# Performance work log

Hardware: AMD Instinct MI355X
Metric: run time of the kernel (lower is better)

Reference implementation:

```python
import jax, jax.numpy as jnp
import numpy as np

B, D, ND, N2, H = 16384, 512, 4, 32, 4
C = D  # attention channels (per-detector feature dim)
EPS = 1e-5


def setup_inputs() -> dict:
    key = jax.random.key(0)
    ks = jax.random.split(key, 8)
    rn = lambda k, s, sc: jax.random.normal(k, s, jnp.float32) * sc
    return {
        'x': jax.random.normal(ks[0], (B, D), jnp.float32),
        'bn1_g': jnp.ones(D * ND, jnp.float32), 'bn1_b': jnp.zeros(D * ND, jnp.float32),
        'w1': rn(ks[1], (ND, D, D), 1e-4),  # diagonal blocks of the masked EnsembleLinear weight
        'bn2_g': jnp.ones(D * ND, jnp.float32), 'bn2_b': jnp.zeros(D * ND, jnp.float32),
        'wq': rn(ks[2], (C, D), 0.02), 'bq': jnp.zeros(C, jnp.float32),
        'wk': rn(ks[3], (C, D), 0.02), 'bk': jnp.zeros(C, jnp.float32),
        'wv': rn(ks[4], (C, D), 0.02), 'bv': jnp.zeros(C, jnp.float32),
        'wo': rn(ks[5], (C, C), 0.02), 'bo': jnp.zeros(C, jnp.float32),
        'ln1_g': jnp.ones(C, jnp.float32), 'ln1_b': jnp.zeros(C, jnp.float32),
        'wff': rn(ks[6], (C, C), 0.02), 'bff': jnp.zeros(C, jnp.float32),
        'ln2_g': jnp.ones(C, jnp.float32), 'ln2_b': jnp.zeros(C, jnp.float32),
        'w2': rn(ks[7], (ND, N2, D), 1e-4),
        'bn3_g': jnp.ones(N2 * ND, jnp.float32), 'bn3_b': jnp.zeros(N2 * ND, jnp.float32),
    }


def _batchnorm(x, g, b):
    # training-mode BatchNorm1d: biased batch stats over the batch axis
    m = x.mean(0)
    v = ((x - m) ** 2).mean(0)
    return (x - m) * jax.lax.rsqrt(v + EPS) * g + b


def _layernorm(x, g, b):
    m = x.mean(-1, keepdims=True)
    v = ((x - m) ** 2).mean(-1, keepdims=True)
    return (x - m) * jax.lax.rsqrt(v + EPS) * g + b


def reference(x, bn1_g, bn1_b, w1, bn2_g, bn2_b, wq, bq, wk, bk, wv, bv, wo, bo,
              ln1_g, ln1_b, wff, bff, ln2_g, ln2_b, w2, bn3_g, bn3_b):
    n = x.shape[0]
    # concat x num_detectors times along features: [n, ND*D]
    xc = jnp.tile(x, (1, ND))
    h = _batchnorm(xc, bn1_g, bn1_b)
    # EnsembleLinear 1: block-diagonal masked matmul == one small GEMM per detector
    h = jnp.einsum('ndi,doi->ndo', h.reshape(n, ND, D), w1).reshape(n, ND * D)
    h = jax.nn.sigmoid(_batchnorm(h, bn2_g, bn2_b))
    # 4-token self-attention over detectors: t is [n, ND, D]
    t = h.reshape(n, ND, D)
    hd = C // H
    q = (t @ wq.T + bq).reshape(n, ND, H, hd).transpose(0, 2, 1, 3)  # [n,H,S,hd]
    k = (t @ wk.T + bk).reshape(n, ND, H, hd).transpose(0, 2, 1, 3)
    v = (t @ wv.T + bv).reshape(n, ND, H, hd).transpose(0, 2, 1, 3)
    scale = jnp.sqrt(jnp.float32(C / H))
    scores = jnp.einsum('nhqd,nhkd->nhqk', q, k) / scale
    attn = jax.nn.softmax(scores, axis=-1)
    o = jnp.einsum('nhqk,nhkd->nhqd', attn, v).transpose(0, 2, 1, 3).reshape(n, ND, C)
    o = o @ wo.T + bo
    a1 = _layernorm(o + t, ln1_g, ln1_b)
    a2 = _layernorm(a1 @ wff.T + bff + a1, ln2_g, ln2_b)
    # EnsembleLinear 2: per-detector D -> N2
    h2 = jnp.einsum('ndi,doi->ndo', a2, w2).reshape(n, ND * N2)
    out = jax.nn.sigmoid(_batchnorm(h2, bn3_g, bn3_b))
    return out
```

## Files before the change

kernel.cpp:

```cpp
#include <hip/hip_runtime.h>
#include <hip/hip_bf16.h>

#define EPS 1e-5f

typedef __attribute__((ext_vector_type(8))) short bf16x8;
typedef __attribute__((ext_vector_type(4))) float f32x4;
typedef __attribute__((ext_vector_type(4))) float float4v;

__device__ __forceinline__ float b2f(short u) {
    union { unsigned int i; float f; } x;
    x.i = ((unsigned int)(unsigned short)u) << 16;
    return x.f;
}
__device__ __forceinline__ short f2b(float f) {
    unsigned int x = __builtin_bit_cast(unsigned int, f);
    unsigned int r = (x + 0x7FFFu + ((x >> 16) & 1u)) >> 16;
    return (short)r;
}

__device__ __forceinline__ void load_lds16(const void* g, void* l) {
    __builtin_amdgcn_global_load_lds(
        (const __attribute__((address_space(1))) unsigned int*)g,
        (__attribute__((address_space(3))) unsigned int*)l, 16, 0, 0);
}


__global__ __launch_bounds__(256) void k_cast_bf16(const float* __restrict__ src,
                                                   short* __restrict__ dst, int n8) {
    int i = blockIdx.x * 256 + threadIdx.x;
    if (i >= n8) return;
    const float4v* s = (const float4v*)src;
    float4v a = s[(long)i * 2], b = s[(long)i * 2 + 1];
    bf16x8 o;
    o[0] = f2b(a[0]); o[1] = f2b(a[1]); o[2] = f2b(a[2]); o[3] = f2b(a[3]);
    o[4] = f2b(b[0]); o[5] = f2b(b[1]); o[6] = f2b(b[2]); o[7] = f2b(b[3]);
    *(bf16x8*)(dst + (long)i * 8) = o;
}

__global__ void k_concat3(const float* __restrict__ a, const float* __restrict__ b,
                          const float* __restrict__ c, float* __restrict__ dst) {
    int i = blockIdx.x * 256 + threadIdx.x;
    if (i < 512) dst[i] = a[i];
    else if (i < 1024) dst[i] = b[i - 512];
    else if (i < 1536) dst[i] = c[i - 1024];
}

__global__ __launch_bounds__(256) void k_statcast_x(const float* __restrict__ x,
                                                    short* __restrict__ xb,
                                                    float* __restrict__ psum, float* __restrict__ psq) {
    int b = blockIdx.x, tid = threadIdx.x;
    const float* xp = x + (long)b * 64 * 512;
    short* xo = xb + (long)b * 64 * 512;
    float s0 = 0, q0 = 0, s1 = 0, q1 = 0;
    for (int r = 0; r < 64; ++r) {
        float v0 = xp[r * 512 + tid];
        float v1 = xp[r * 512 + tid + 256];
        xo[r * 512 + tid] = f2b(v0);
        xo[r * 512 + tid + 256] = f2b(v1);
        s0 += v0; q0 += v0 * v0; s1 += v1; q1 += v1 * v1;
    }
    psum[b * 512 + tid] = s0; psum[b * 512 + tid + 256] = s1;
    psq[b * 512 + tid] = q0;  psq[b * 512 + tid + 256] = q1;
}


__global__ __launch_bounds__(256) void k_finalize_meanrs(const float* __restrict__ psum,
                                                         const float* __restrict__ psq,
                                                         int nparts, int ncols, float invB,
                                                         float* __restrict__ mean, float* __restrict__ rs) {
    int l = threadIdx.x & 63, grp = threadIdx.x >> 6;
    int c = blockIdx.x * 64 + l;
    float s = 0, q = 0;
    for (int p = grp; p < nparts; p += 4) {
        s += psum[(long)p * ncols + c];
        q += psq[(long)p * ncols + c];
    }
    __shared__ float rs_[4][64], rq_[4][64];
    rs_[grp][l] = s; rq_[grp][l] = q;
    __syncthreads();
    if (grp == 0) {
        s = rs_[0][l] + rs_[1][l] + rs_[2][l] + rs_[3][l];
        q = rq_[0][l] + rq_[1][l] + rq_[2][l] + rq_[3][l];
        float m = s * invB;
        float v = q * invB - m * m;
        mean[c] = m;
        rs[c] = rsqrtf(v + EPS);
    }
}

__global__ __launch_bounds__(256) void k_finalize_ss(const float* __restrict__ psum,
                                                     const float* __restrict__ psq,
                                                     int nparts, int ncols, float invB,
                                                     const float* __restrict__ g, const float* __restrict__ bb,
                                                     float* __restrict__ scale, float* __restrict__ shift) {
    int l = threadIdx.x & 63, grp = threadIdx.x >> 6;
    int c = blockIdx.x * 64 + l;
    float s = 0, q = 0;
    for (int p = grp; p < nparts; p += 4) {
        s += psum[(long)p * ncols + c];
        q += psq[(long)p * ncols + c];
    }
    __shared__ float rs_[4][64], rq_[4][64];
    rs_[grp][l] = s; rq_[grp][l] = q;
    __syncthreads();
    if (grp == 0) {
        s = rs_[0][l] + rs_[1][l] + rs_[2][l] + rs_[3][l];
        q = rq_[0][l] + rq_[1][l] + rq_[2][l] + rq_[3][l];
        float m = s * invB, v = q * invB - m * m;
        float sc = g[c] * rsqrtf(v + EPS);
        scale[c] = sc;
        shift[c] = bb[c] - m * sc;
    }
}

__global__ __launch_bounds__(256) void k_fold_w1(const float* __restrict__ w1, const float* __restrict__ g1,
                                                 const float* __restrict__ b1, const float* __restrict__ mean,
                                                 const float* __restrict__ rs,
                                                 short* __restrict__ W1b, float* __restrict__ beff) {
    int bx = blockIdx.x;
    int d = bx >> 9, tid = threadIdx.x;
    const float* wrow = w1 + (long)bx * 512;
    float part = 0.f;
    for (int i = tid; i < 512; i += 256) {
        float wv = wrow[i];
        float sc = rs[i] * g1[d * 512 + i];
        W1b[(long)bx * 512 + i] = f2b(wv * sc);
        part += (b1[d * 512 + i] - mean[i] * sc) * wv;
    }
    __shared__ float red[256];
    red[tid] = part;
    __syncthreads();
    for (int st = 128; st > 0; st >>= 1) {
        if (tid < st) red[tid] += red[tid + st];
        __syncthreads();
    }
    if (tid == 0) beff[bx] = red[0];
}

__global__ __launch_bounds__(256) void k_bnsig(const short* h, short* t,
                                               const float* __restrict__ scale,
                                               const float* __restrict__ shift) {
    long i8 = ((long)blockIdx.x * 256 + threadIdx.x) * 8;
    int c0 = (int)(i8 & 2047);
    bf16x8 v = *(const bf16x8*)(h + i8);
    bf16x8 o;
#pragma unroll
    for (int j = 0; j < 8; ++j) {
        float x = b2f(v[j]) * scale[c0 + j] + shift[c0 + j];
        o[j] = f2b(1.f / (1.f + __expf(-x)));
    }
    *(bf16x8*)(t + i8) = o;
}

__global__ __launch_bounds__(256) void k_ln(const short* in, short* out,
                                            const float* __restrict__ g, const float* __restrict__ bb) {
    int w = threadIdx.x >> 6, lane = threadIdx.x & 63;
    long row = (long)blockIdx.x * 4 + w;
    const short* rp = in + row * 512;
    bf16x8 v = *(const bf16x8*)(rp + lane * 8);
    float f[8];
    float s = 0.f;
#pragma unroll
    for (int j = 0; j < 8; ++j) { f[j] = b2f(v[j]); s += f[j]; }
#pragma unroll
    for (int m = 1; m < 64; m <<= 1) s += __shfl_xor(s, m, 64);
    float mean = s * (1.f / 512.f);
    float q = 0.f;
#pragma unroll
    for (int j = 0; j < 8; ++j) { float d = f[j] - mean; q += d * d; }
#pragma unroll
    for (int m = 1; m < 64; m <<= 1) q += __shfl_xor(q, m, 64);
    float rs = rsqrtf(q * (1.f / 512.f) + EPS);
    bf16x8 o;
#pragma unroll
    for (int j = 0; j < 8; ++j) {
        int c = lane * 8 + j;
        o[j] = f2b((f[j] - mean) * rs * g[c] + bb[c]);
    }
    *(bf16x8*)(out + row * 512 + lane * 8) = o;
}

__global__ __launch_bounds__(256) void k_stats_o(const float* __restrict__ pre,
                                                 float* __restrict__ psum, float* __restrict__ psq) {
    int b = blockIdx.x, tid = threadIdx.x;
    int c = tid & 127, rh = tid >> 7;
    const float* pp = pre + (long)b * 128 * 128;
    float s = 0, q = 0;
    for (int r = rh; r < 128; r += 2) {
        float v = pp[r * 128 + c];
        s += v; q += v * v;
    }
    psum[(b * 2 + rh) * 128 + c] = s;
    psq[(b * 2 + rh) * 128 + c] = q;
}

__global__ __launch_bounds__(256) void k_bn3sig(const float* __restrict__ pre, float* __restrict__ out,
                                                const float* __restrict__ scale, const float* __restrict__ shift) {
    long i4 = ((long)blockIdx.x * 256 + threadIdx.x) * 4;
    float4v v = *(const float4v*)(pre + i4);
    int c0 = (int)(i4 & 127);
    float4v o;
#pragma unroll
    for (int j = 0; j < 4; ++j) {
        float x = v[j] * scale[c0 + j] + shift[c0 + j];
        o[j] = 1.f / (1.f + __expf(-x));
    }
    *(float4v*)(out + i4) = o;
}


template <int BM, int BN, int WGM, int WGN, bool ADD_RES, bool OUT_BF16>
__global__ __launch_bounds__(WGM* WGN * 64) void k_gemm_bt(
    const short* __restrict__ A, int a_zoff, int lda,
    const short* __restrict__ W, int w_zoff,
    const float* __restrict__ bias, int bias_zoff,
    short* __restrict__ Cb, float* __restrict__ Cf, int c_zoff, int ldc,
    const short* __restrict__ R, int ldr, int K) {
    constexpr int BK = 32;
    constexpr int WM = BM / WGM, WN = BN / WGN;
    constexpr int AM = WM / 16, AN = WN / 16;
    constexpr int NT = WGM * WGN * 64;
    constexpr int CH = (BM + BN) * (BK / 8);

    __shared__ alignas(16) short Smem[(BM + BN) * BK];

    int tid = threadIdx.x;
    int wave = tid >> 6, lane = tid & 63;
    int wm = (wave % WGM) * WM, wn = (wave / WGM) * WN;
    long m0 = (long)blockIdx.x * BM;
    int n0 = blockIdx.y * BN;
    int z = blockIdx.z;
    const short* Az = A + (long)z * a_zoff;
    const short* Wz = W + (long)z * w_zoff;

    f32x4 acc[AM][AN];
#pragma unroll
    for (int i = 0; i < AM; ++i)
#pragma unroll
        for (int j = 0; j < AN; ++j)
#pragma unroll
            for (int q = 0; q < 4; ++q) acc[i][j][q] = 0.f;

    int fr = lane & 15, ko = (lane >> 4) * 8;

    for (int k0 = 0; k0 < K; k0 += BK) {
#pragma unroll
        for (int c = tid; c < CH; c += NT) {
            int row = c >> 2, koff = (c & 3) * 8;
            const short* g = (row < BM) ? (Az + (m0 + row) * lda + k0 + koff)
                                        : (Wz + (long)(n0 + row - BM) * K + k0 + koff);
            load_lds16(g, (char*)Smem + (size_t)c * 16);
        }
        __syncthreads();
        bf16x8 af[AM], bfr[AN];
#pragma unroll
        for (int i = 0; i < AM; ++i) af[i] = *(const bf16x8*)(&Smem[(wm + i * 16 + fr) * BK + ko]);
#pragma unroll
        for (int j = 0; j < AN; ++j) bfr[j] = *(const bf16x8*)(&Smem[(BM + wn + j * 16 + fr) * BK + ko]);
#pragma unroll
        for (int i = 0; i < AM; ++i)
#pragma unroll
            for (int j = 0; j < AN; ++j)
                acc[i][j] = __builtin_amdgcn_mfma_f32_16x16x32_bf16(af[i], bfr[j], acc[i][j], 0, 0, 0);
        __syncthreads();
    }

    int cr = (lane >> 4) * 4, cc = lane & 15;
#pragma unroll
    for (int i = 0; i < AM; ++i) {
#pragma unroll
        for (int j = 0; j < AN; ++j) {
            int col = n0 + wn + j * 16 + cc;
            float bv = bias ? bias[(long)z * bias_zoff + col] : 0.f;
#pragma unroll
            for (int q = 0; q < 4; ++q) {
                long row = m0 + wm + i * 16 + cr + q;
                float v = acc[i][j][q] + bv;
                if constexpr (ADD_RES) v += b2f(R[row * (long)ldr + col]);
                long idx = row * (long)ldc + (long)z * c_zoff + col;
                if constexpr (OUT_BF16) Cb[idx] = f2b(v);
                else Cf[idx] = v;
            }
        }
    }
}


__global__ __launch_bounds__(256) void k_gemm_e1(
    const short* __restrict__ A, const short* __restrict__ W1, const float* __restrict__ beff,
    short* __restrict__ h, float* __restrict__ psum, float* __restrict__ psq) {
    constexpr int BK = 32;
    __shared__ alignas(16) short Smem[256 * BK];
    __shared__ float cS[2][128], cQ[2][128];

    int tid = threadIdx.x;
    int wave = tid >> 6, lane = tid & 63;
    int wm = (wave & 1) * 64, wn = (wave >> 1) * 64;
    long m0 = (long)blockIdx.x * 128;
    int n0 = blockIdx.y * 128;
    int z = blockIdx.z;
    const short* Wz = W1 + (long)z * 512 * 512;

    f32x4 acc[4][4];
#pragma unroll
    for (int i = 0; i < 4; ++i)
#pragma unroll
        for (int j = 0; j < 4; ++j)
#pragma unroll
            for (int q = 0; q < 4; ++q) acc[i][j][q] = 0.f;

    int fr = lane & 15, ko = (lane >> 4) * 8;

    for (int k0 = 0; k0 < 512; k0 += BK) {
#pragma unroll
        for (int c = tid; c < 1024; c += 256) {
            int row = c >> 2, koff = (c & 3) * 8;
            const short* g = (row < 128) ? (A + (m0 + row) * 512 + k0 + koff)
                                         : (Wz + (long)(n0 + row - 128) * 512 + k0 + koff);
            load_lds16(g, (char*)Smem + (size_t)c * 16);
        }
        __syncthreads();
        bf16x8 af[4], bfr[4];
#pragma unroll
        for (int i = 0; i < 4; ++i) af[i] = *(const bf16x8*)(&Smem[(wm + i * 16 + fr) * BK + ko]);
#pragma unroll
        for (int j = 0; j < 4; ++j) bfr[j] = *(const bf16x8*)(&Smem[(128 + wn + j * 16 + fr) * BK + ko]);
#pragma unroll
        for (int i = 0; i < 4; ++i)
#pragma unroll
            for (int j = 0; j < 4; ++j)
                acc[i][j] = __builtin_amdgcn_mfma_f32_16x16x32_bf16(af[i], bfr[j], acc[i][j], 0, 0, 0);
        __syncthreads();
    }

    int cr = (lane >> 4) * 4, cc = lane & 15;
    float bv[4], colS[4], colQ[4];
#pragma unroll
    for (int j = 0; j < 4; ++j) {
        bv[j] = beff[z * 512 + n0 + wn + j * 16 + cc];
        colS[j] = 0.f; colQ[j] = 0.f;
    }
#pragma unroll
    for (int i = 0; i < 4; ++i)
#pragma unroll
        for (int j = 0; j < 4; ++j)
#pragma unroll
            for (int q = 0; q < 4; ++q) {
                float v = acc[i][j][q] + bv[j];
                acc[i][j][q] = v;
                colS[j] += v; colQ[j] += v * v;
            }
#pragma unroll
    for (int i = 0; i < 4; ++i)
#pragma unroll
        for (int q = 0; q < 4; ++q) {
            long row = m0 + wm + i * 16 + cr + q;
            short* hp = h + row * 2048 + z * 512 + n0 + wn + cc;
#pragma unroll
            for (int j = 0; j < 4; ++j) hp[j * 16] = f2b(acc[i][j][q]);
        }
#pragma unroll
    for (int j = 0; j < 4; ++j) {
        float s = colS[j], qq = colQ[j];
        s += __shfl_xor(s, 16, 64); s += __shfl_xor(s, 32, 64);
        qq += __shfl_xor(qq, 16, 64); qq += __shfl_xor(qq, 32, 64);
        if (lane < 16) { cS[wave & 1][wn + j * 16 + cc] = s; cQ[wave & 1][wn + j * 16 + cc] = qq; }
    }
    __syncthreads();
    if (tid < 128) {
        float S = cS[0][tid] + cS[1][tid];
        float Q = cQ[0][tid] + cQ[1][tid];
        psum[(long)blockIdx.x * 2048 + z * 512 + n0 + tid] = S;
        psq[(long)blockIdx.x * 2048 + z * 512 + n0 + tid] = Q;
    }
}

__global__ __launch_bounds__(256) void k_attn(const short* __restrict__ qkv, short* __restrict__ ao) {
    __shared__ alignas(16) short lds[4][4][1544];
    __shared__ float attn_s[4][4][4][4];
    int w = threadIdx.x >> 6, lane = threadIdx.x & 63;
    long n = (long)blockIdx.x * 4 + w;
    const short* src = qkv + n * 4 * 1536;
#pragma unroll
    for (int c = 0; c < 12; ++c) {
        int e = c * 512 + lane * 8;
        *(bf16x8*)(&lds[w][e / 1536][e % 1536]) = *(const bf16x8*)(src + e);
    }
    __syncthreads();
    int h = lane >> 4, a = (lane >> 2) & 3, b = lane & 3;
    const short* qp = &lds[w][a][h * 128];
    const short* kp = &lds[w][b][512 + h * 128];
    float s = 0.f;
#pragma unroll
    for (int j = 0; j < 128; j += 8) {
        bf16x8 qv = *(const bf16x8*)(qp + j);
        bf16x8 kv = *(const bf16x8*)(kp + j);
#pragma unroll
        for (int x = 0; x < 8; ++x) s += b2f(qv[x]) * b2f(kv[x]);
    }
    s *= 0.08838834764831845f;
    float mx = fmaxf(s, __shfl_xor(s, 1, 64));
    mx = fmaxf(mx, __shfl_xor(mx, 2, 64));
    float e = __expf(s - mx);
    float den = e + __shfl_xor(e, 1, 64);
    den += __shfl_xor(den, 2, 64);
    attn_s[w][h][a][b] = e / den;
    __syncthreads();
    int ta = lane >> 4, cg = lane & 15;
#pragma unroll
    for (int hh = 0; hh < 4; ++hh) {
        int c0 = hh * 128 + cg * 8;
        float at0 = attn_s[w][hh][ta][0], at1 = attn_s[w][hh][ta][1];
        float at2 = attn_s[w][hh][ta][2], at3 = attn_s[w][hh][ta][3];
        bf16x8 v0 = *(const bf16x8*)(&lds[w][0][1024 + c0]);
        bf16x8 v1 = *(const bf16x8*)(&lds[w][1][1024 + c0]);
        bf16x8 v2 = *(const bf16x8*)(&lds[w][2][1024 + c0]);
        bf16x8 v3 = *(const bf16x8*)(&lds[w][3][1024 + c0]);
        bf16x8 ov;
#pragma unroll
        for (int j = 0; j < 8; ++j) {
            float val = at0 * b2f(v0[j]) + at1 * b2f(v1[j]) + at2 * b2f(v2[j]) + at3 * b2f(v3[j]);
            ov[j] = f2b(val);
        }
        *(bf16x8*)(ao + (n * 4 + ta) * 512 + c0) = ov;
    }
}


extern "C" void kernel_launch(void* const* d_in, const int* in_sizes, int n_in,
                              void* d_out, int out_size, void* d_ws, size_t ws_size,
                              hipStream_t stream) {
    const float* x = (const float*)d_in[0];
    const float* bn1_g = (const float*)d_in[1];
    const float* bn1_b = (const float*)d_in[2];
    const float* w1 = (const float*)d_in[3];
    const float* bn2_g = (const float*)d_in[4];
    const float* bn2_b = (const float*)d_in[5];
    const float* wq = (const float*)d_in[6];
    const float* bq = (const float*)d_in[7];
    const float* wk = (const float*)d_in[8];
    const float* bk = (const float*)d_in[9];
    const float* wv = (const float*)d_in[10];
    const float* bv = (const float*)d_in[11];
    const float* wo = (const float*)d_in[12];
    const float* bo = (const float*)d_in[13];
    const float* ln1_g = (const float*)d_in[14];
    const float* ln1_b = (const float*)d_in[15];
    const float* wff = (const float*)d_in[16];
    const float* bff = (const float*)d_in[17];
    const float* ln2_g = (const float*)d_in[18];
    const float* ln2_b = (const float*)d_in[19];
    const float* w2 = (const float*)d_in[20];
    const float* bn3_g = (const float*)d_in[21];
    const float* bn3_b = (const float*)d_in[22];
    float* out = (float*)d_out;

    char* ws = (char*)d_ws;
    size_t off = 0;
    auto alloc = [&](size_t bytes) {
        void* p = ws + off;
        off = (off + bytes + 255) & ~(size_t)255;
        return p;
    };

    short* W1b = (short*)alloc(4l * 512 * 512 * 2);
    float* beff = (float*)alloc(4l * 512 * 4);
    short* Wqkvb = (short*)alloc(1536l * 512 * 2);
    float* bqkv = (float*)alloc(1536l * 4);
    short* wo_b = (short*)alloc(512l * 512 * 2);
    short* wff_b = (short*)alloc(512l * 512 * 2);
    short* w2_b = (short*)alloc(4l * 32 * 512 * 2);
    float* mean1 = (float*)alloc(512 * 4);
    float* rs1 = (float*)alloc(512 * 4);
    float* scale2 = (float*)alloc(2048 * 4);
    float* shift2 = (float*)alloc(2048 * 4);
    float* scale3 = (float*)alloc(128 * 4);
    float* shift3 = (float*)alloc(128 * 4);
    float* psum1 = (float*)alloc(256l * 512 * 4);
    float* psq1 = (float*)alloc(256l * 512 * 4);
    float* psum2 = (float*)alloc(128l * 2048 * 4);
    float* psq2 = (float*)alloc(128l * 2048 * 4);
    float* psum3 = (float*)alloc(256l * 128 * 4);
    float* psq3 = (float*)alloc(256l * 128 * 4);
    short* slotA = (short*)alloc(16384l * 2048 * 2);
    float* out_pre = (float*)alloc(16384l * 128 * 4);

    long NC = 1024;
    for (long cand = 8192; cand >= 1024; cand >>= 1) {
        if (off + (size_t)cand * 24576 + (1u << 20) <= ws_size) { NC = cand; break; }
    }
    char* arena = (char*)alloc((size_t)NC * 24576);
    short* xb = (short*)arena;
    short* qkv_c = (short*)arena;
    short* attn_c = (short*)(arena + (size_t)NC * 12288);
    short* a1_c = attn_c + (size_t)NC * 2048;
    short* a2_c = a1_c + (size_t)NC * 2048;

    dim3 B256(256);

    hipLaunchKernelGGL(k_statcast_x, dim3(256), B256, 0, stream, x, xb, psum1, psq1);
    hipLaunchKernelGGL(k_cast_bf16, dim3(128), B256, 0, stream, wq, Wqkvb, 262144 / 8);
    hipLaunchKernelGGL(k_cast_bf16, dim3(128), B256, 0, stream, wk, Wqkvb + 262144, 262144 / 8);
    hipLaunchKernelGGL(k_cast_bf16, dim3(128), B256, 0, stream, wv, Wqkvb + 524288, 262144 / 8);
    hipLaunchKernelGGL(k_cast_bf16, dim3(128), B256, 0, stream, wo, wo_b, 262144 / 8);
    hipLaunchKernelGGL(k_cast_bf16, dim3(128), B256, 0, stream, wff, wff_b, 262144 / 8);
    hipLaunchKernelGGL(k_cast_bf16, dim3(32), B256, 0, stream, w2, w2_b, 65536 / 8);
    hipLaunchKernelGGL(k_concat3, dim3(6), B256, 0, stream, bq, bk, bv, bqkv);

    hipLaunchKernelGGL(k_finalize_meanrs, dim3(8), B256, 0, stream, psum1, psq1, 256, 512,
                       1.f / 16384.f, mean1, rs1);
    hipLaunchKernelGGL(k_fold_w1, dim3(2048), B256, 0, stream, w1, bn1_g, bn1_b, mean1, rs1, W1b, beff);

    hipLaunchKernelGGL(k_gemm_e1, dim3(128, 4, 4), B256, 0, stream,
                       xb, W1b, beff, slotA, psum2, psq2);

    hipLaunchKernelGGL(k_finalize_ss, dim3(32), B256, 0, stream, psum2, psq2, 128, 2048,
                       1.f / 16384.f, bn2_g, bn2_b, scale2, shift2);
    hipLaunchKernelGGL(k_bnsig, dim3(16384), B256, 0, stream, slotA, slotA, scale2, shift2);

    long nch = 16384 / NC;
    for (long c = 0; c < nch; ++c) {
        long r0 = c * NC;
        const short* t_c = slotA + r0 * 2048;
        int gx = (int)(NC * 4 / 128);

        hipLaunchKernelGGL((k_gemm_bt<128, 128, 2, 2, false, true>), dim3(gx, 12, 1), B256, 0, stream,
                           t_c, 0, 512, Wqkvb, 0, bqkv, 0,
                           qkv_c, (float*)nullptr, 0, 1536, (const short*)nullptr, 0, 512);

        hipLaunchKernelGGL(k_attn, dim3((int)(NC / 4)), B256, 0, stream, qkv_c, attn_c);

        hipLaunchKernelGGL((k_gemm_bt<128, 128, 2, 2, true, true>), dim3(gx, 4, 1), B256, 0, stream,
                           attn_c, 0, 512, wo_b, 0, bo, 0,
                           a1_c, (float*)nullptr, 0, 512, t_c, 512, 512);

        hipLaunchKernelGGL(k_ln, dim3((int)NC), B256, 0, stream, a1_c, a1_c, ln1_g, ln1_b);

        hipLaunchKernelGGL((k_gemm_bt<128, 128, 2, 2, true, true>), dim3(gx, 4, 1), B256, 0, stream,
                           a1_c, 0, 512, wff_b, 0, bff, 0,
                           a2_c, (float*)nullptr, 0, 512, a1_c, 512, 512);

        hipLaunchKernelGGL(k_ln, dim3((int)NC), B256, 0, stream, a2_c, a2_c, ln2_g, ln2_b);

        hipLaunchKernelGGL((k_gemm_bt<128, 32, 4, 1, false, false>), dim3((int)(NC / 128), 1, 4), B256, 0, stream,
                           a2_c, 512, 2048, w2_b, 32 * 512, (const float*)nullptr, 0,
                           (short*)nullptr, out_pre + r0 * 128, 32, 128, (const short*)nullptr, 0, 512);
    }

    hipLaunchKernelGGL(k_stats_o, dim3(128), B256, 0, stream, out_pre, psum3, psq3);
    hipLaunchKernelGGL(k_finalize_ss, dim3(2), B256, 0, stream, psum3, psq3, 256, 128,
                       1.f / 16384.f, bn3_g, bn3_b, scale3, shift3);
    hipLaunchKernelGGL(k_bn3sig, dim3(2048), B256, 0, stream, out_pre, out, scale3, shift3);
}
```

Measured before the change: 629.0 us.

## Add 256x256 double-buffered MFMA GEMM kernel for attention-block projections

Adds a new GEMM kernel with 256x256 output tiles, 8 waves per block, and double-buffered async global-to-LDS loads. K-steps of 64 are pipelined with explicit waitcnt and barriers, and setprio is raised around the MFMA loop. A workgroup remap groups blocks for L2 locality. It replaces the 128x128 kernel for the QKV, output and feed-forward projections to get more data reuse per tile and to overlap loads with compute. In exchange the tile is larger, so there are fewer blocks per chunk, register pressure is higher and occupancy is one block per CU.

```diff
diff --git a/kernel.cpp b/kernel.cpp
--- a/kernel.cpp
+++ b/kernel.cpp
@@ -206,6 +206,108 @@
         o[j] = 1.f / (1.f + __expf(-x));
     }
     *(float4v*)(out + i4) = o;
+}
+
+
+template <bool ADD_RES>
+__global__ __launch_bounds__(512, 1) void k_gemm256(
+    const short* __restrict__ A, int lda,
+    const short* __restrict__ W,
+    const float* __restrict__ bias,
+    const short* R, int ldr,
+    short* __restrict__ C, int ldc, int NT) {
+    constexpr int PANEL = 4112;
+    __shared__ alignas(16) char lds[2][2][8 * PANEL];
+
+    int tid = threadIdx.x, wave = tid >> 6, lane = tid & 63;
+    int nwg = gridDim.x;
+    int wg = (nwg & 7) == 0 ? (blockIdx.x & 7) * (nwg >> 3) + (blockIdx.x >> 3)
+                            : blockIdx.x;
+    int nt = wg % NT, mt = wg / NT;
+    long m0 = (long)mt * 256;
+    int n0 = nt * 256;
+    int wm = (wave & 1) * 128, wn = (wave >> 1) * 64;
+    int fr = lane & 15, hi = lane >> 4;
+
+    f32x4 acc[8][4];
+#pragma unroll
+    for (int mi = 0; mi < 8; ++mi)
+#pragma unroll
+        for (int ni = 0; ni < 4; ++ni)
+#pragma unroll
+            for (int q = 0; q < 4; ++q) acc[mi][ni][q] = 0.f;
+
+    auto stage = [&](int b, int k0) {
+#pragma unroll
+        for (int i = 0; i < 4; ++i) {
+            int c = tid + i * 512, p = c >> 8, r = c & 255;
+            load_lds16(A + (m0 + r) * lda + k0 + p * 8, &lds[b][0][p * PANEL + r * 16]);
+        }
+#pragma unroll
+        for (int i = 0; i < 4; ++i) {
+            int c = tid + i * 512, p = c >> 8, r = c & 255;
+            load_lds16(W + (long)(n0 + r) * 512 + k0 + p * 8, &lds[b][1][p * PANEL + r * 16]);
+        }
+    };
+
+    stage(0, 0);
+    stage(1, 64);
+
+    for (int t = 0; t < 8; ++t) {
+        int b = t & 1;
+        if (t < 7) asm volatile("s_waitcnt vmcnt(8)" ::: "memory");
+        else       asm volatile("s_waitcnt vmcnt(0)" ::: "memory");
+        __builtin_amdgcn_s_barrier();
+        asm volatile("" ::: "memory");
+
+        bf16x8 af[2][8], bf[2][4];
+#pragma unroll
+        for (int kk = 0; kk < 2; ++kk) {
+            int p = kk * 4 + hi;
+#pragma unroll
+            for (int mi = 0; mi < 8; ++mi)
+                af[kk][mi] = *(const bf16x8*)&lds[b][0][p * PANEL + (wm + mi * 16 + fr) * 16];
+#pragma unroll
+            for (int ni = 0; ni < 4; ++ni)
+                bf[kk][ni] = *(const bf16x8*)&lds[b][1][p * PANEL + (wn + ni * 16 + fr) * 16];
+        }
+        asm volatile("s_waitcnt lgkmcnt(0)" ::: "memory");
+        __builtin_amdgcn_s_barrier();
+        asm volatile("" ::: "memory");
+
+        if (t < 6) stage(b, (t + 2) * 64);
+
+        __builtin_amdgcn_s_setprio(1);
+#pragma unroll
+        for (int kk = 0; kk < 2; ++kk)
+#pragma unroll
+            for (int mi = 0; mi < 8; ++mi)
+#pragma unroll
+                for (int ni = 0; ni < 4; ++ni)
+                    acc[mi][ni] = __builtin_amdgcn_mfma_f32_16x16x32_bf16(
+                        af[kk][mi], bf[kk][ni], acc[mi][ni], 0, 0, 0);
+        __builtin_amdgcn_s_setprio(0);
+    }
+
+    int cr = hi * 4, cc = fr;
+    float bv[4];
+#pragma unroll
+    for (int ni = 0; ni < 4; ++ni) bv[ni] = bias[n0 + wn + ni * 16 + cc];
+#pragma unroll
+    for (int mi = 0; mi < 8; ++mi) {
+#pragma unroll
+        for (int q = 0; q < 4; ++q) {
+            long row = m0 + wm + mi * 16 + cr + q;
+            short* cp = C + row * (long)ldc + n0 + wn + cc;
+            const short* rp = ADD_RES ? (R + row * (long)ldr + n0 + wn + cc) : nullptr;
+#pragma unroll
+            for (int ni = 0; ni < 4; ++ni) {
+                float v = acc[mi][ni][q] + bv[ni];
+                if constexpr (ADD_RES) v += b2f(rp[ni * 16]);
+                cp[ni * 16] = f2b(v);
+            }
+        }
+    }
 }
 
 
@@ -522,23 +624,23 @@
     for (long c = 0; c < nch; ++c) {
         long r0 = c * NC;
         const short* t_c = slotA + r0 * 2048;
-        int gx = (int)(NC * 4 / 128);
-
-        hipLaunchKernelGGL((k_gemm_bt<128, 128, 2, 2, false, true>), dim3(gx, 12, 1), B256, 0, stream,
-                           t_c, 0, 512, Wqkvb, 0, bqkv, 0,
-                           qkv_c, (float*)nullptr, 0, 1536, (const short*)nullptr, 0, 512);
+        int mtiles = (int)(NC * 4 / 256);
+
+        hipLaunchKernelGGL((k_gemm256<false>), dim3(mtiles * 6), dim3(512), 0, stream,
+                           t_c, 512, Wqkvb, bqkv, (const short*)nullptr, 0,
+                           qkv_c, 1536, 6);
 
         hipLaunchKernelGGL(k_attn, dim3((int)(NC / 4)), B256, 0, stream, qkv_c, attn_c);
 
-        hipLaunchKernelGGL((k_gemm_bt<128, 128, 2, 2, true, true>), dim3(gx, 4, 1), B256, 0, stream,
-                           attn_c, 0, 512, wo_b, 0, bo, 0,
-                           a1_c, (float*)nullptr, 0, 512, t_c, 512, 512);
+        hipLaunchKernelGGL((k_gemm256<true>), dim3(mtiles * 2), dim3(512), 0, stream,
+                           attn_c, 512, wo_b, bo, t_c, 512,
+                           a1_c, 512, 2);
 
         hipLaunchKernelGGL(k_ln, dim3((int)NC), B256, 0, stream, a1_c, a1_c, ln1_g, ln1_b);
 
-        hipLaunchKernelGGL((k_gemm_bt<128, 128, 2, 2, true, true>), dim3(gx, 4, 1), B256, 0, stream,
-                           a1_c, 0, 512, wff_b, 0, bff, 0,
-                           a2_c, (float*)nullptr, 0, 512, a1_c, 512, 512);
+        hipLaunchKernelGGL((k_gemm256<true>), dim3(mtiles * 2), dim3(512), 0, stream,
+                           a1_c, 512, wff_b, bff, a1_c, 512,
+                           a2_c, 512, 2);
 
         hipLaunchKernelGGL(k_ln, dim3((int)NC), B256, 0, stream, a2_c, a2_c, ln2_g, ln2_b);
 
```

Result: slower. 1.001 ms (+59.2%).

## Unchunk post-attention GEMMs and LN over full batch; fuse weight prep kernels

Applied to the files above, without the earlier changes.

Adds a full-size scratch buffer so that only the QKV GEMM and attention stay chunked, while the output projection, both LayerNorms, the FFN and the final ensemble GEMM each run once over all 16384 rows with in-place aliasing (restrict removed from C and R). It also merges the six weight casts and the bias concat into a single prep kernel. The intent is fewer launches and larger grids that fill the GPU better. The cost is a larger workspace, and the intermediates may no longer stay in cache between stages.

```diff
diff --git a/kernel.cpp b/kernel.cpp
--- a/kernel.cpp
+++ b/kernel.cpp
@@ -25,24 +25,42 @@
 }
 
 
-__global__ __launch_bounds__(256) void k_cast_bf16(const float* __restrict__ src,
-                                                   short* __restrict__ dst, int n8) {
-    int i = blockIdx.x * 256 + threadIdx.x;
-    if (i >= n8) return;
+__device__ __forceinline__ void cast8(const float* __restrict__ src, short* __restrict__ dst, long idx) {
     const float4v* s = (const float4v*)src;
-    float4v a = s[(long)i * 2], b = s[(long)i * 2 + 1];
+    float4v a = s[idx * 2], b = s[idx * 2 + 1];
     bf16x8 o;
     o[0] = f2b(a[0]); o[1] = f2b(a[1]); o[2] = f2b(a[2]); o[3] = f2b(a[3]);
     o[4] = f2b(b[0]); o[5] = f2b(b[1]); o[6] = f2b(b[2]); o[7] = f2b(b[3]);
-    *(bf16x8*)(dst + (long)i * 8) = o;
-}
-
-__global__ void k_concat3(const float* __restrict__ a, const float* __restrict__ b,
-                          const float* __restrict__ c, float* __restrict__ dst) {
-    int i = blockIdx.x * 256 + threadIdx.x;
-    if (i < 512) dst[i] = a[i];
-    else if (i < 1024) dst[i] = b[i - 512];
-    else if (i < 1536) dst[i] = c[i - 1024];
+    *(bf16x8*)(dst + idx * 8) = o;
+}
+
+__global__ __launch_bounds__(256) void k_prep(
+    const float* __restrict__ wq, const float* __restrict__ wk, const float* __restrict__ wv,
+    const float* __restrict__ wo, const float* __restrict__ wff, const float* __restrict__ w2,
+    const float* __restrict__ bq, const float* __restrict__ bk, const float* __restrict__ bv,
+    short* __restrict__ Wqkvb, short* __restrict__ wo_b, short* __restrict__ wff_b,
+    short* __restrict__ w2_b, float* __restrict__ bqkv) {
+    int bid = blockIdx.x, tid = threadIdx.x;
+    if (bid < 640) {
+        int seg = bid >> 7;
+        long idx = (long)(bid & 127) * 256 + tid;
+        const float* src;
+        short* dst;
+        if (seg == 0) { src = wq; dst = Wqkvb; }
+        else if (seg == 1) { src = wk; dst = Wqkvb + 262144; }
+        else if (seg == 2) { src = wv; dst = Wqkvb + 524288; }
+        else if (seg == 3) { src = wo; dst = wo_b; }
+        else { src = wff; dst = wff_b; }
+        cast8(src, dst, idx);
+    } else if (bid < 672) {
+        long idx = (long)(bid - 640) * 256 + tid;
+        cast8(w2, w2_b, idx);
+    } else {
+        int i = (bid - 672) * 256 + tid;
+        if (i < 512) bqkv[i] = bq[i];
+        else if (i < 1024) bqkv[i] = bk[i - 512];
+        else if (i < 1536) bqkv[i] = bv[i - 1024];
+    }
 }
 
 __global__ __launch_bounds__(256) void k_statcast_x(const float* __restrict__ x,
@@ -214,8 +232,8 @@
     const short* __restrict__ A, int a_zoff, int lda,
     const short* __restrict__ W, int w_zoff,
     const float* __restrict__ bias, int bias_zoff,
-    short* __restrict__ Cb, float* __restrict__ Cf, int c_zoff, int ldc,
-    const short* __restrict__ R, int ldr, int K) {
+    short* Cb, float* Cf, int c_zoff, int ldc,
+    const short* R, int ldr, int K) {
     constexpr int BK = 32;
     constexpr int WM = BM / WGM, WN = BN / WGN;
     constexpr int AM = WM / 16, AN = WN / 16;
@@ -484,28 +502,23 @@
     float* psq3 = (float*)alloc(256l * 128 * 4);
     short* slotA = (short*)alloc(16384l * 2048 * 2);
     float* out_pre = (float*)alloc(16384l * 128 * 4);
-
-    long NC = 1024;
-    for (long cand = 8192; cand >= 1024; cand >>= 1) {
-        if (off + (size_t)cand * 24576 + (1u << 20) <= ws_size) { NC = cand; break; }
-    }
-    char* arena = (char*)alloc((size_t)NC * 24576);
+    short* bufB = (short*)alloc(16384l * 2048 * 2);
+
+    long NCq = 1024;
+    for (long cand = 4096; cand >= 1024; cand >>= 1) {
+        if (off + (size_t)cand * 12288 + (1u << 20) <= ws_size) { NCq = cand; break; }
+    }
+    char* arena = (char*)alloc((size_t)NCq * 12288);
     short* xb = (short*)arena;
     short* qkv_c = (short*)arena;
-    short* attn_c = (short*)(arena + (size_t)NC * 12288);
-    short* a1_c = attn_c + (size_t)NC * 2048;
-    short* a2_c = a1_c + (size_t)NC * 2048;
+    xb = bufB;
 
     dim3 B256(256);
 
+    hipLaunchKernelGGL(k_prep, dim3(678), B256, 0, stream,
+                       wq, wk, wv, wo, wff, w2, bq, bk, bv,
+                       Wqkvb, wo_b, wff_b, w2_b, bqkv);
     hipLaunchKernelGGL(k_statcast_x, dim3(256), B256, 0, stream, x, xb, psum1, psq1);
-    hipLaunchKernelGGL(k_cast_bf16, dim3(128), B256, 0, stream, wq, Wqkvb, 262144 / 8);
-    hipLaunchKernelGGL(k_cast_bf16, dim3(128), B256, 0, stream, wk, Wqkvb + 262144, 262144 / 8);
-    hipLaunchKernelGGL(k_cast_bf16, dim3(128), B256, 0, stream, wv, Wqkvb + 524288, 262144 / 8);
-    hipLaunchKernelGGL(k_cast_bf16, dim3(128), B256, 0, stream, wo, wo_b, 262144 / 8);
-    hipLaunchKernelGGL(k_cast_bf16, dim3(128), B256, 0, stream, wff, wff_b, 262144 / 8);
-    hipLaunchKernelGGL(k_cast_bf16, dim3(32), B256, 0, stream, w2, w2_b, 65536 / 8);
-    hipLaunchKernelGGL(k_concat3, dim3(6), B256, 0, stream, bq, bk, bv, bqkv);
 
     hipLaunchKernelGGL(k_finalize_meanrs, dim3(8), B256, 0, stream, psum1, psq1, 256, 512,
                        1.f / 16384.f, mean1, rs1);
@@ -518,34 +531,35 @@
                        1.f / 16384.f, bn2_g, bn2_b, scale2, shift2);
     hipLaunchKernelGGL(k_bnsig, dim3(16384), B256, 0, stream, slotA, slotA, scale2, shift2);
 
-    long nch = 16384 / NC;
+    long nch = 16384 / NCq;
     for (long c = 0; c < nch; ++c) {
-        long r0 = c * NC;
+        long r0 = c * NCq;
         const short* t_c = slotA + r0 * 2048;
-        int gx = (int)(NC * 4 / 128);
+        int gx = (int)(NCq * 4 / 128);
 
         hipLaunchKernelGGL((k_gemm_bt<128, 128, 2, 2, false, true>), dim3(gx, 12, 1), B256, 0, stream,
                            t_c, 0, 512, Wqkvb, 0, bqkv, 0,
                            qkv_c, (float*)nullptr, 0, 1536, (const short*)nullptr, 0, 512);
 
-        hipLaunchKernelGGL(k_attn, dim3((int)(NC / 4)), B256, 0, stream, qkv_c, attn_c);
-
-        hipLaunchKernelGGL((k_gemm_bt<128, 128, 2, 2, true, true>), dim3(gx, 4, 1), B256, 0, stream,
-                           attn_c, 0, 512, wo_b, 0, bo, 0,
-                           a1_c, (float*)nullptr, 0, 512, t_c, 512, 512);
-
-        hipLaunchKernelGGL(k_ln, dim3((int)NC), B256, 0, stream, a1_c, a1_c, ln1_g, ln1_b);
-
-        hipLaunchKernelGGL((k_gemm_bt<128, 128, 2, 2, true, true>), dim3(gx, 4, 1), B256, 0, stream,
-                           a1_c, 0, 512, wff_b, 0, bff, 0,
-                           a2_c, (float*)nullptr, 0, 512, a1_c, 512, 512);
-
-        hipLaunchKernelGGL(k_ln, dim3((int)NC), B256, 0, stream, a2_c, a2_c, ln2_g, ln2_b);
-
-        hipLaunchKernelGGL((k_gemm_bt<128, 32, 4, 1, false, false>), dim3((int)(NC / 128), 1, 4), B256, 0, stream,
-                           a2_c, 512, 2048, w2_b, 32 * 512, (const float*)nullptr, 0,
-                           (short*)nullptr, out_pre + r0 * 128, 32, 128, (const short*)nullptr, 0, 512);
-    }
+        hipLaunchKernelGGL(k_attn, dim3((int)(NCq / 4)), B256, 0, stream,
+                           qkv_c, bufB + r0 * 2048);
+    }
+
+    hipLaunchKernelGGL((k_gemm_bt<128, 128, 2, 2, true, true>), dim3(512, 4, 1), B256, 0, stream,
+                       bufB, 0, 512, wo_b, 0, bo, 0,
+                       slotA, (float*)nullptr, 0, 512, slotA, 512, 512);
+
+    hipLaunchKernelGGL(k_ln, dim3(16384), B256, 0, stream, slotA, slotA, ln1_g, ln1_b);
+
+    hipLaunchKernelGGL((k_gemm_bt<128, 128, 2, 2, true, true>), dim3(512, 4, 1), B256, 0, stream,
+                       slotA, 0, 512, wff_b, 0, bff, 0,
+                       bufB, (float*)nullptr, 0, 512, slotA, 512, 512);
+
+    hipLaunchKernelGGL(k_ln, dim3(16384), B256, 0, stream, bufB, bufB, ln2_g, ln2_b);
+
+    hipLaunchKernelGGL((k_gemm_bt<128, 32, 4, 1, false, false>), dim3(128, 1, 4), B256, 0, stream,
+                       bufB, 512, 2048, w2_b, 32 * 512, (const float*)nullptr, 0,
+                       (short*)nullptr, out_pre, 32, 128, (const short*)nullptr, 0, 512);
 
     hipLaunchKernelGGL(k_stats_o, dim3(128), B256, 0, stream, out_pre, psum3, psq3);
     hipLaunchKernelGGL(k_finalize_ss, dim3(2), B256, 0, stream, psum3, psq3, 256, 128,
```

Result: no change. 618.1 us (-1.7%).
